# Kernel tuning notes

Measured on AMD Instinct MI355X. Metric: run time of the kernel, lower is better.

Reference implementation:

```python
import jax, jax.numpy as jnp
import numpy as np

N, E, H, NODE_IN, EDGE_DIM, L = 10000, 400000, 128, 6, 3, 4
LN_EPS = 1e-5


def _lin_init(key, fan_in, fan_out):
    return jax.random.normal(key, (fan_in, fan_out), dtype=jnp.float32) / np.sqrt(fan_in)


def setup_inputs() -> dict:
    key = jax.random.key(0)
    ks = jax.random.split(key, 24)
    x = jax.random.normal(ks[0], (N, NODE_IN), dtype=jnp.float32)
    edge_index = jax.random.randint(ks[1], (2, E), 0, N, dtype=jnp.int64)
    edge_attr = jax.random.normal(ks[2], (E, EDGE_DIM), dtype=jnp.float32)
    # encoder
    enc_w1 = _lin_init(ks[3], NODE_IN, H); enc_b1 = jnp.zeros((H,), jnp.float32)
    enc_w2 = _lin_init(ks[4], H, H); enc_b2 = jnp.zeros((H,), jnp.float32)
    # per-layer stacked params [L, ...]
    msg_w1 = jax.vmap(lambda k: _lin_init(k, 2 * H + EDGE_DIM, H))(jax.random.split(ks[5], L))
    msg_b1 = jnp.zeros((L, H), jnp.float32)
    msg_w2 = jax.vmap(lambda k: _lin_init(k, H, H))(jax.random.split(ks[6], L))
    msg_b2 = jnp.zeros((L, H), jnp.float32)
    upd_w1 = jax.vmap(lambda k: _lin_init(k, 2 * H, H))(jax.random.split(ks[7], L))
    upd_b1 = jnp.zeros((L, H), jnp.float32)
    upd_w2 = jax.vmap(lambda k: _lin_init(k, H, H))(jax.random.split(ks[8], L))
    upd_b2 = jnp.zeros((L, H), jnp.float32)
    ln_g = jnp.ones((L, H), jnp.float32)
    ln_b = jnp.zeros((L, H), jnp.float32)
    # decoder
    dec_w1 = _lin_init(ks[9], H, H); dec_b1 = jnp.zeros((H,), jnp.float32)
    dec_w2 = _lin_init(ks[10], H, 1); dec_b2 = jnp.zeros((1,), jnp.float32)
    return dict(x=x, edge_index=edge_index, edge_attr=edge_attr,
                enc_w1=enc_w1, enc_b1=enc_b1, enc_w2=enc_w2, enc_b2=enc_b2,
                msg_w1=msg_w1, msg_b1=msg_b1, msg_w2=msg_w2, msg_b2=msg_b2,
                upd_w1=upd_w1, upd_b1=upd_b1, upd_w2=upd_w2, upd_b2=upd_b2,
                ln_g=ln_g, ln_b=ln_b,
                dec_w1=dec_w1, dec_b1=dec_b1, dec_w2=dec_w2, dec_b2=dec_b2)


def _layernorm(h, g, b):
    mu = jnp.mean(h, axis=-1, keepdims=True)
    var = jnp.mean(jnp.square(h - mu), axis=-1, keepdims=True)
    return (h - mu) * jax.lax.rsqrt(var + LN_EPS) * g + b


def reference(x, edge_index, edge_attr,
              enc_w1, enc_b1, enc_w2, enc_b2,
              msg_w1, msg_b1, msg_w2, msg_b2,
              upd_w1, upd_b1, upd_w2, upd_b2,
              ln_g, ln_b,
              dec_w1, dec_b1, dec_w2, dec_b2):
    src, tgt = edge_index[0], edge_index[1]  # PyG default flow: message from x_j=src to x_i=tgt
    # in-degree counts for mean aggregation (zero-degree nodes -> 0 output, like scatter_mean)
    counts = jax.ops.segment_sum(jnp.ones((E,), jnp.float32), tgt, num_segments=N)
    inv_counts = (1.0 / jnp.maximum(counts, 1.0))[:, None]
    # encoder
    h = jax.nn.relu(x @ enc_w1 + enc_b1) @ enc_w2 + enc_b2  # [N, H]
    for l in range(L):
        x_i = h[tgt]  # [E, H] target features
        x_j = h[src]  # [E, H] source features
        m_in = jnp.concatenate([x_i, x_j, edge_attr], axis=-1)  # [E, 2H+edge_dim]
        m = jax.nn.relu(m_in @ msg_w1[l] + msg_b1[l]) @ msg_w2[l] + msg_b2[l]  # [E, H]
        agg = jax.ops.segment_sum(m, tgt, num_segments=N) * inv_counts  # [N, H] mean aggregate
        u_in = jnp.concatenate([h, agg], axis=-1)  # [N, 2H]
        u = jax.nn.relu(u_in @ upd_w1[l] + upd_b1[l]) @ upd_w2[l] + upd_b2[l]
        h = _layernorm(u + h, ln_g[l], ln_b[l])  # residual (in==out channels)
    # decoder
    return jax.nn.relu(h @ dec_w1 + dec_b1) @ dec_w2 + dec_b2  # [N, 1]
```

## Files before the change

kernel.cpp:

```cpp
#include <hip/hip_runtime.h>

#define NN 10000
#define NE 400000
#define HD 128
#define NIN 6
#define EDIM 3
#define NL 4
#define CAP 96
#define LN_EPS 1e-5f

typedef unsigned short u16;
using short8 = __attribute__((ext_vector_type(8))) short;
using f32x4 = __attribute__((ext_vector_type(4))) float;

__device__ __forceinline__ u16 f2bf(float x) {
    unsigned u = __float_as_uint(x);
    return (u16)((u + 0x7fff + ((u >> 16) & 1)) >> 16);
}
__device__ __forceinline__ float bf2f(u16 h) { return __uint_as_float(((unsigned)h) << 16); }
__device__ __forceinline__ void split2(float x, u16& hi, u16& lo) {
    hi = f2bf(x);
    lo = f2bf(x - bf2f(hi));
}
#define MFMA(a, b, c) __builtin_amdgcn_mfma_f32_16x16x32_bf16((a), (b), (c), 0, 0, 0)


__global__ __launch_bounds__(256) void k_prep(
    const float* __restrict__ msg_w2, const float* __restrict__ msg_b2, const float* __restrict__ upd_w1,
    const float* __restrict__ upd_w2, const float* __restrict__ msg_w1, const float* __restrict__ dec_w1,
    const float* __restrict__ enc_w2, float* __restrict__ M2, float* __restrict__ c2, int* __restrict__ cnt,
    u16* __restrict__ fG2, u16* __restrict__ fPQ, u16* __restrict__ fDec, u16* __restrict__ fEnc) {
    int idx = blockIdx.x * 256 + threadIdx.x;
    if (idx < 65536) {
        int l = idx >> 14, rem = idx & 16383, i = rem >> 7, jj = rem & 127;
        const float* U1b = upd_w1 + (size_t)l * 2 * HD * HD + (size_t)HD * HD;
        const float* W2 = msg_w2 + (size_t)l * HD * HD + (size_t)i * HD;
        float acc = 0.f;
        for (int t = 0; t < HD; ++t) acc += W2[t] * U1b[(size_t)t * HD + jj];
        M2[idx] = acc;
    } else if (idx < 66048) {
        int r = idx - 65536;
        int l = r >> 7, jj = r & 127;
        const float* U1b = upd_w1 + (size_t)l * 2 * HD * HD + (size_t)HD * HD;
        const float* b2 = msg_b2 + l * HD;
        float acc = 0.f;
        for (int t = 0; t < HD; ++t) acc += b2[t] * U1b[(size_t)t * HD + jj];
        c2[r] = acc;
    } else if (idx < 76048) {
        cnt[idx - 66048] = 0;
    } else if (idx < 84240) {
        int gg = idx - 76048;
        int l = gg >> 11, r = gg & 2047;
        int ct = r >> 8, ks = (r >> 6) & 3, lane = r & 63;
        int n = ct * 16 + (lane & 15), kb = ks * 32 + ((lane >> 4) << 3);
        u16* dst = fG2 + (size_t)gg * 8;
        const float* W = upd_w2 + (size_t)l * 128 * 128;
#pragma unroll
        for (int j = 0; j < 8; ++j) dst[j] = f2bf(W[(size_t)(kb + j) * 128 + n]);
    } else if (idx < 100624) {
        int gg = idx - 84240;
        int li = gg >> 12, r = gg & 4095;
        int ct = r >> 8, ks = (r >> 6) & 3, lane = r & 63;
        int n = ct * 16 + (lane & 15), kb = ks * 32 + ((lane >> 4) << 3);
        u16* dst = fPQ + (size_t)gg * 8;
        const float* W = msg_w1 + (size_t)li * (2 * HD + EDIM) * HD;
#pragma unroll
        for (int j = 0; j < 8; ++j) {
            int k = kb + j;
            float v = (n < 128) ? W[(size_t)k * 128 + n] : W[(size_t)(128 + k) * 128 + (n - 128)];
            dst[j] = f2bf(v);
        }
    } else if (idx < 102672) {
        int r = idx - 100624;
        int ct = r >> 8, ks = (r >> 6) & 3, lane = r & 63;
        int n = ct * 16 + (lane & 15), kb = ks * 32 + ((lane >> 4) << 3);
        u16* dst = fDec + (size_t)r * 8;
#pragma unroll
        for (int j = 0; j < 8; ++j) dst[j] = f2bf(dec_w1[(size_t)(kb + j) * 128 + n]);
    } else if (idx < 104720) {
        int r = idx - 102672;
        int ct = r >> 8, ks = (r >> 6) & 3, lane = r & 63;
        int n = ct * 16 + (lane & 15), kb = ks * 32 + ((lane >> 4) << 3);
        u16* dst = fEnc + (size_t)r * 8;
#pragma unroll
        for (int j = 0; j < 8; ++j) dst[j] = f2bf(enc_w2[(size_t)(kb + j) * 128 + n]);
    }
}


__global__ __launch_bounds__(256) void k_scatfrag(
    const int* __restrict__ src, const int* __restrict__ tgt, const float* __restrict__ ea,
    int* __restrict__ cnt, float4* __restrict__ sea,
    const float* __restrict__ upd_w1, const float* __restrict__ M2, u16* __restrict__ fG1) {
    if (blockIdx.x < 64) {
        int g = blockIdx.x * 256 + threadIdx.x;
        int l = g >> 12, r = g & 4095;
        int ct = r >> 9, ks = (r >> 6) & 7, lane = r & 63;
        int n = ct * 16 + (lane & 15), kb = ks * 32 + ((lane >> 4) << 3);
        u16* dst = fG1 + (size_t)g * 8;
        const float* U = upd_w1 + (size_t)l * 256 * 128;
        const float* Ml = M2 + (size_t)l * 128 * 128;
#pragma unroll
        for (int j = 0; j < 8; ++j) {
            int k = kb + j;
            float v = (k < 128) ? U[(size_t)k * 128 + n] : Ml[(size_t)(k - 128) * 128 + n];
            dst[j] = f2bf(v);
        }
    } else {
        int e = (blockIdx.x - 64) * 256 + threadIdx.x;
        if (e >= NE) return;
        int t = tgt[e];
        int pos = atomicAdd(&cnt[t], 1);
        if (pos < CAP) {
            sea[t * CAP + pos] =
                make_float4(ea[e * 3], ea[e * 3 + 1], ea[e * 3 + 2], __uint_as_float((unsigned)src[e]));
        }
    }
}


__global__ __launch_bounds__(512) void k_enc(const float* __restrict__ x, const float* __restrict__ ew1,
                                             const float* __restrict__ eb1, const u16* __restrict__ fEnc,
                                             const float* __restrict__ eb2, const u16* __restrict__ fPQ0,
                                             const float* __restrict__ mb1, u16* __restrict__ h_hi,
                                             u16* __restrict__ h_lo, float* __restrict__ PQf,
                                             u16* __restrict__ Qb) {
    __shared__ u16 tHi[2048], tLo[2048];
    int tid = threadIdx.x, w = tid >> 6, lane = tid & 63, q = lane >> 4, c = lane & 15;
    int band = blockIdx.x * 16;
    {
        int col = w * 16 + c;
        float wv[NIN];
#pragma unroll
        for (int k = 0; k < NIN; ++k) wv[k] = ew1[k * HD + col];
        float ebv = eb1[col];
#pragma unroll
        for (int reg = 0; reg < 4; ++reg) {
            int row = band + q * 4 + reg;
            float t = ebv;
#pragma unroll
            for (int k = 0; k < NIN; ++k) t += x[(size_t)row * NIN + k] * wv[k];
            t = fmaxf(t, 0.f);
            u16 hi, lo;
            split2(t, hi, lo);
            int r16 = q * 4 + reg;
            int a = r16 * 128 + (((col >> 3) ^ r16) << 3) + (col & 7);
            tHi[a] = hi;
            tLo[a] = lo;
        }
    }
    __syncthreads();
    short8 aH[4], aL[4];
#pragma unroll
    for (int ks = 0; ks < 4; ++ks) {
        int a = c * 128 + (((ks * 4 + q) ^ c) << 3);
        aH[ks] = *(const short8*)&tHi[a];
        aL[ks] = *(const short8*)&tLo[a];
    }
    f32x4 acc = {0, 0, 0, 0};
    {
        const u16* fb = fEnc + (size_t)w * 4 * 512 + lane * 8;
#pragma unroll
        for (int ks = 0; ks < 4; ++ks) {
            short8 b = *(const short8*)(fb + ks * 512);
            acc = MFMA(aH[ks], b, acc);
            acc = MFMA(aL[ks], b, acc);
        }
    }
    __syncthreads();
    {
        int col = w * 16 + c;
        float ebv = eb2[col];
#pragma unroll
        for (int reg = 0; reg < 4; ++reg) {
            int r16 = q * 4 + reg, row = band + r16;
            float hval = acc[reg] + ebv;
            u16 hi, lo;
            split2(hval, hi, lo);
            h_hi[(size_t)row * HD + col] = hi;
            h_lo[(size_t)row * HD + col] = lo;
            int a = r16 * 128 + (((col >> 3) ^ r16) << 3) + (col & 7);
            tHi[a] = hi;
            tLo[a] = lo;
        }
    }
    __syncthreads();
#pragma unroll
    for (int ks = 0; ks < 4; ++ks) {
        int a = c * 128 + (((ks * 4 + q) ^ c) << 3);
        aH[ks] = *(const short8*)&tHi[a];
        aL[ks] = *(const short8*)&tLo[a];
    }
#pragma unroll
    for (int i = 0; i < 2; ++i) {
        int ctg = w * 2 + i;
        const u16* fb = fPQ0 + (size_t)ctg * 4 * 512 + lane * 8;
        f32x4 a3 = {0, 0, 0, 0};
#pragma unroll
        for (int ks = 0; ks < 4; ++ks) {
            short8 b = *(const short8*)(fb + ks * 512);
            a3 = MFMA(aH[ks], b, a3);
            a3 = MFMA(aL[ks], b, a3);
        }
        int col = ctg * 16 + c;
        if (ctg < 8) {
            float bias = mb1[col];
#pragma unroll
            for (int reg = 0; reg < 4; ++reg)
                PQf[(size_t)(band + q * 4 + reg) * HD + col] = a3[reg] + bias;
        } else {
            int colq = col - 128;
#pragma unroll
            for (int reg = 0; reg < 4; ++reg)
                Qb[(size_t)(band + q * 4 + reg) * HD + colq] = f2bf(a3[reg]);
        }
    }
}


template <bool LAST>
__global__ __launch_bounds__(512) void k_layer(
    const float* __restrict__ PQf_in, const u16* __restrict__ Qb_in,
    const int* __restrict__ cnt, const float4* __restrict__ sea, const float* __restrict__ wc,
    u16* __restrict__ h_hi, u16* __restrict__ h_lo,
    const u16* __restrict__ fG1, const u16* __restrict__ fG2,
    const float* __restrict__ ub1, const float* __restrict__ c2l, const float* __restrict__ ub2,
    const float* __restrict__ g, const float* __restrict__ bb,
    const u16* __restrict__ fPQ, const float* __restrict__ nb1,
    float* __restrict__ PQf_out, u16* __restrict__ Qb_out,
    const u16* __restrict__ fDec, const float* __restrict__ db1, const float* __restrict__ dw2,
    const float* __restrict__ db2, float* __restrict__ out) {
    __shared__ u16 sHi[2048], sLo[2048];
    __shared__ u16 tHi[2048], tLo[2048];
    __shared__ float red[8][8][2];
    int tid = threadIdx.x, w = tid >> 6, lane = tid & 63, q = lane >> 4, c = lane & 15;
    int band = blockIdx.x * 8;
    int j = lane * 2;
    {
        float2 wcr0 = *(const float2*)(wc + j);
        float2 wcr1 = *(const float2*)(wc + HD + j);
        float2 wcr2 = *(const float2*)(wc + 2 * HD + j);
        int n = __builtin_amdgcn_readfirstlane(band + w);
        int cn = cnt[n];
        float invn = 1.0f / fmaxf((float)cn, 1.0f);
        int cle = __builtin_amdgcn_readfirstlane(cn < CAP ? cn : CAP);
        float2 p = *(const float2*)(PQf_in + (size_t)n * HD + j);
        float acc0 = 0.f, acc1 = 0.f;
        const float4* bucket = sea + (size_t)n * CAP;
        auto edge1 = [&](float4 A) {
            int sv = (int)__float_as_uint(A.w);
            float c0 = A.x * wcr0.x + A.y * wcr1.x + A.z * wcr2.x;
            float c1 = A.x * wcr0.y + A.y * wcr1.y + A.z * wcr2.y;
            unsigned u = *(const unsigned*)(Qb_in + (size_t)sv * HD + j);
            acc0 += fmaxf(p.x + __uint_as_float(u << 16) + c0, 0.f);
            acc1 += fmaxf(p.y + __uint_as_float(u & 0xffff0000u) + c1, 0.f);
        };
        int e = 0;
        for (; e + 3 < cle; e += 4) {
            float4 A0 = bucket[e], A1 = bucket[e + 1], A2 = bucket[e + 2], A3 = bucket[e + 3];
            edge1(A0);
            edge1(A1);
            edge1(A2);
            edge1(A3);
        }
        for (; e < cle; ++e) edge1(bucket[e]);
        float v0 = acc0 * invn, v1 = acc1 * invn;
        u16 h0, l0, h1, l1;
        split2(v0, h0, l0);
        split2(v1, h1, l1);
        int a = w * 128 + (((j >> 3) ^ w) << 3) + (j & 7);
        *(ushort2*)&sHi[a] = make_ushort2(h0, h1);
        *(ushort2*)&sLo[a] = make_ushort2(l0, l1);
    }
    __syncthreads();
    f32x4 acc = {0, 0, 0, 0};
    {
        const u16* fb = fG1 + (size_t)w * 8 * 512 + lane * 8;
        size_t rb = (size_t)(band + c) * HD + q * 8;
#pragma unroll
        for (int ks = 0; ks < 4; ++ks) {
            short8 aH = *(const short8*)(h_hi + rb + ks * 32);
            short8 aL = *(const short8*)(h_lo + rb + ks * 32);
            short8 b = *(const short8*)(fb + ks * 512);
            acc = MFMA(aH, b, acc);
            acc = MFMA(aL, b, acc);
        }
#pragma unroll
        for (int ks = 0; ks < 4; ++ks) {
            int a = c * 128 + (((ks * 4 + q) ^ c) << 3);
            short8 aH = *(const short8*)&sHi[a];
            short8 aL = *(const short8*)&sLo[a];
            short8 b = *(const short8*)(fb + (4 + ks) * 512);
            acc = MFMA(aH, b, acc);
            acc = MFMA(aL, b, acc);
        }
    }
    float alv[4];
#pragma unroll
    for (int reg = 0; reg < 4; ++reg) alv[reg] = (cnt[band + ((q * 4 + reg) & 7)] > 0) ? 1.f : 0.f;
    {
        int col = w * 16 + c;
        float u1b = ub1[col], cc = c2l[col];
#pragma unroll
        for (int reg = 0; reg < 4; ++reg) {
            int r16 = q * 4 + reg;
            float t = fmaxf(acc[reg] + u1b + alv[reg] * cc, 0.f);
            u16 hi, lo;
            split2(t, hi, lo);
            int a = r16 * 128 + (((col >> 3) ^ r16) << 3) + (col & 7);
            tHi[a] = hi;
            tLo[a] = lo;
        }
    }
    __syncthreads();
    f32x4 acc2 = {0, 0, 0, 0};
    {
        const u16* fb = fG2 + (size_t)w * 4 * 512 + lane * 8;
#pragma unroll
        for (int ks = 0; ks < 4; ++ks) {
            int a = c * 128 + (((ks * 4 + q) ^ c) << 3);
            short8 aH = *(const short8*)&tHi[a];
            short8 aL = *(const short8*)&tLo[a];
            short8 b = *(const short8*)(fb + ks * 512);
            acc2 = MFMA(aH, b, acc2);
            acc2 = MFMA(aL, b, acc2);
        }
    }
    float vv[4];
    {
        int col = w * 16 + c;
        float u2b = ub2[col];
#pragma unroll
        for (int reg = 0; reg < 4; ++reg) {
            int r16 = q * 4 + reg;
            size_t idx = (size_t)(band + (r16 & 7)) * HD + col;
            float hres = bf2f(h_hi[idx]) + bf2f(h_lo[idx]);
            vv[reg] = acc2[reg] + u2b + hres;
        }
    }
#pragma unroll
    for (int reg = 0; reg < 4; ++reg) {
        float s = vv[reg];
        float s2 = vv[reg] * vv[reg];
        for (int m = 1; m < 16; m <<= 1) {
            s += __shfl_xor(s, m);
            s2 += __shfl_xor(s2, m);
        }
        int r16 = q * 4 + reg;
        if (c == 0 && r16 < 8) {
            red[r16][w][0] = s;
            red[r16][w][1] = s2;
        }
    }
    __syncthreads();
    float mu[4], rs[4];
#pragma unroll
    for (int reg = 0; reg < 4; ++reg) {
        int r16 = q * 4 + reg;
        if (r16 < 8) {
            float S1 = 0.f, S2 = 0.f;
#pragma unroll
            for (int ww = 0; ww < 8; ++ww) {
                S1 += red[r16][ww][0];
                S2 += red[r16][ww][1];
            }
            float m = S1 * (1.f / HD);
            float var = S2 * (1.f / HD) - m * m;
            mu[reg] = m;
            rs[reg] = rsqrtf(var + LN_EPS);
        } else {
            mu[reg] = 0.f;
            rs[reg] = 1.f;
        }
    }
    {
        int col = w * 16 + c;
        float gg = g[col], bv = bb[col];
#pragma unroll
        for (int reg = 0; reg < 4; ++reg) {
            int r16 = q * 4 + reg;
            float o = (vv[reg] - mu[reg]) * rs[reg] * gg + bv;
            u16 hi, lo;
            split2(o, hi, lo);
            int a = r16 * 128 + (((col >> 3) ^ r16) << 3) + (col & 7);
            tHi[a] = hi;
            tLo[a] = lo;
            if (!LAST && r16 < 8) {
                size_t idx = (size_t)(band + r16) * HD + col;
                h_hi[idx] = hi;
                h_lo[idx] = lo;
            }
        }
    }
    __syncthreads();
    short8 aH3[4], aL3[4];
#pragma unroll
    for (int ks = 0; ks < 4; ++ks) {
        int a = c * 128 + (((ks * 4 + q) ^ c) << 3);
        aH3[ks] = *(const short8*)&tHi[a];
        aL3[ks] = *(const short8*)&tLo[a];
    }
    if (!LAST) {
#pragma unroll
        for (int i = 0; i < 2; ++i) {
            int ctg = w * 2 + i;
            const u16* fb = fPQ + (size_t)ctg * 4 * 512 + lane * 8;
            f32x4 a3 = {0, 0, 0, 0};
#pragma unroll
            for (int ks = 0; ks < 4; ++ks) {
                short8 b = *(const short8*)(fb + ks * 512);
                a3 = MFMA(aH3[ks], b, a3);
                a3 = MFMA(aL3[ks], b, a3);
            }
            int col = ctg * 16 + c;
            if (ctg < 8) {
                float bias = nb1[col];
#pragma unroll
                for (int reg = 0; reg < 4; ++reg) {
                    int r16 = q * 4 + reg;
                    if (r16 < 8) PQf_out[(size_t)(band + r16) * HD + col] = a3[reg] + bias;
                }
            } else {
                int colq = col - 128;
#pragma unroll
                for (int reg = 0; reg < 4; ++reg) {
                    int r16 = q * 4 + reg;
                    if (r16 < 8) Qb_out[(size_t)(band + r16) * HD + colq] = f2bf(a3[reg]);
                }
            }
        }
    } else {
        float part[4];
        {
            const u16* fb = fDec + (size_t)w * 4 * 512 + lane * 8;
            f32x4 a3 = {0, 0, 0, 0};
#pragma unroll
            for (int ks = 0; ks < 4; ++ks) {
                short8 b = *(const short8*)(fb + ks * 512);
                a3 = MFMA(aH3[ks], b, a3);
                a3 = MFMA(aL3[ks], b, a3);
            }
            int col = w * 16 + c;
            float w2v = dw2[col], b1v = db1[col];
#pragma unroll
            for (int reg = 0; reg < 4; ++reg) part[reg] = fmaxf(a3[reg] + b1v, 0.f) * w2v;
        }
#pragma unroll
        for (int reg = 0; reg < 4; ++reg) {
            float s = part[reg];
            for (int m = 1; m < 16; m <<= 1) s += __shfl_xor(s, m);
            int r16 = q * 4 + reg;
            if (c == 0 && r16 < 8) red[r16][w][0] = s;
        }
        __syncthreads();
        if (tid < 8) {
            float s = db2[0];
#pragma unroll
            for (int ww = 0; ww < 8; ++ww) s += red[tid][ww][0];
            out[band + tid] = s;
        }
    }
}


extern "C" void kernel_launch(void* const* d_in, const int* in_sizes, int n_in,
                              void* d_out, int out_size, void* d_ws, size_t ws_size,
                              hipStream_t stream) {
    const float* x = (const float*)d_in[0];
    const int* eidx = (const int*)d_in[1];
    const float* eattr = (const float*)d_in[2];
    const float* enc_w1 = (const float*)d_in[3];
    const float* enc_b1 = (const float*)d_in[4];
    const float* enc_w2 = (const float*)d_in[5];
    const float* enc_b2 = (const float*)d_in[6];
    const float* msg_w1 = (const float*)d_in[7];
    const float* msg_b1 = (const float*)d_in[8];
    const float* msg_w2 = (const float*)d_in[9];
    const float* msg_b2 = (const float*)d_in[10];
    const float* upd_w1 = (const float*)d_in[11];
    const float* upd_b1 = (const float*)d_in[12];
    const float* upd_w2 = (const float*)d_in[13];
    const float* upd_b2 = (const float*)d_in[14];
    const float* ln_g = (const float*)d_in[15];
    const float* ln_b = (const float*)d_in[16];
    const float* dec_w1 = (const float*)d_in[17];
    const float* dec_b1 = (const float*)d_in[18];
    const float* dec_w2 = (const float*)d_in[19];
    const float* dec_b2 = (const float*)d_in[20];
    const int* srcp = eidx;
    const int* tgtp = eidx + NE;

    char* base = (char*)d_ws;
    size_t off = 0;
    auto alloc = [&](size_t bytes) -> void* {
        off = (off + 15) & ~(size_t)15;
        void* p = base + off;
        off += bytes;
        return p;
    };
    float4* sea = (float4*)alloc((size_t)NN * CAP * 16);
    float* PQf0 = (float*)alloc((size_t)NN * HD * 4);
    float* PQf1 = (float*)alloc((size_t)NN * HD * 4);
    u16* Qb0 = (u16*)alloc((size_t)NN * HD * 2);
    u16* Qb1 = (u16*)alloc((size_t)NN * HD * 2);
    u16* h_hi = (u16*)alloc((size_t)NN * HD * 2);
    u16* h_lo = (u16*)alloc((size_t)NN * HD * 2);
    int* cnt = (int*)alloc((size_t)NN * 4);
    float* M2 = (float*)alloc((size_t)NL * HD * HD * 4);
    float* c2 = (float*)alloc((size_t)NL * HD * 4);
    u16* fG1 = (u16*)alloc((size_t)131072 * 2);
    u16* fG2 = (u16*)alloc((size_t)65536 * 2);
    u16* fPQ = (u16*)alloc((size_t)131072 * 2);
    u16* fDec = (u16*)alloc((size_t)16384 * 2);
    u16* fEnc = (u16*)alloc((size_t)16384 * 2);

    k_prep<<<410, 256, 0, stream>>>(msg_w2, msg_b2, upd_w1, upd_w2, msg_w1, dec_w1, enc_w2,
                                    M2, c2, cnt, fG2, fPQ, fDec, fEnc);
    k_scatfrag<<<64 + (NE + 255) / 256, 256, 0, stream>>>(srcp, tgtp, eattr, cnt, sea, upd_w1, M2, fG1);
    k_enc<<<NN / 16, 512, 0, stream>>>(x, enc_w1, enc_b1, fEnc, enc_b2, fPQ, msg_b1, h_hi, h_lo, PQf0, Qb0);

    float* PQin = PQf0;
    u16* Qin = Qb0;
    float* PQout = PQf1;
    u16* Qout = Qb1;
    for (int l = 0; l < NL; ++l) {
        const float* wc = msg_w1 + (size_t)l * (2 * HD + EDIM) * HD + (size_t)2 * HD * HD;
        if (l < NL - 1) {
            k_layer<false><<<NN / 8, 512, 0, stream>>>(
                PQin, Qin, cnt, sea, wc, h_hi, h_lo,
                fG1 + (size_t)l * 32768, fG2 + (size_t)l * 16384,
                upd_b1 + l * HD, c2 + l * HD, upd_b2 + l * HD, ln_g + l * HD, ln_b + l * HD,
                fPQ + (size_t)(l + 1) * 32768, msg_b1 + (size_t)(l + 1) * HD, PQout, Qout,
                nullptr, nullptr, nullptr, nullptr, nullptr);
        } else {
            k_layer<true><<<NN / 8, 512, 0, stream>>>(
                PQin, Qin, cnt, sea, wc, h_hi, h_lo,
                fG1 + (size_t)l * 32768, fG2 + (size_t)l * 16384,
                upd_b1 + l * HD, c2 + l * HD, upd_b2 + l * HD, ln_g + l * HD, ln_b + l * HD,
                nullptr, nullptr, nullptr, nullptr,
                fDec, dec_b1, dec_w2, dec_b2, (float*)d_out);
        }
        float* tf = PQin; PQin = PQout; PQout = tf;
        u16* tq = Qin; Qin = Qout; Qout = tq;
    }
}
```

Before: 310.7 us.

## Process 16 nodes per layer block with split-edge gather per wave

Each layer block now handles 16 nodes instead of 8, so all 16 rows of the 16x16 MFMA tiles hold real data and the row masks go away. Each wave aggregates two nodes; within a wave the two 32-lane halves take alternate edges, each lane reads 4 columns, and the halves are combined with a cross-half shuffle. The aim is to stop wasting half of every MFMA tile and to make the gather loads wider and more parallel. In exchange, the grid is half as large, which lowers occupancy and the number of blocks available to hide gather latency.

```diff
diff --git a/kernel.cpp b/kernel.cpp
--- a/kernel.cpp
+++ b/kernel.cpp
@@ -232,45 +232,77 @@
     const float* __restrict__ db2, float* __restrict__ out) {
     __shared__ u16 sHi[2048], sLo[2048];
     __shared__ u16 tHi[2048], tLo[2048];
-    __shared__ float red[8][8][2];
+    __shared__ float red[16][8][2];
     int tid = threadIdx.x, w = tid >> 6, lane = tid & 63, q = lane >> 4, c = lane & 15;
-    int band = blockIdx.x * 8;
-    int j = lane * 2;
-    {
-        float2 wcr0 = *(const float2*)(wc + j);
-        float2 wcr1 = *(const float2*)(wc + HD + j);
-        float2 wcr2 = *(const float2*)(wc + 2 * HD + j);
-        int n = __builtin_amdgcn_readfirstlane(band + w);
-        int cn = cnt[n];
-        float invn = 1.0f / fmaxf((float)cn, 1.0f);
-        int cle = __builtin_amdgcn_readfirstlane(cn < CAP ? cn : CAP);
-        float2 p = *(const float2*)(PQf_in + (size_t)n * HD + j);
-        float acc0 = 0.f, acc1 = 0.f;
-        const float4* bucket = sea + (size_t)n * CAP;
-        auto edge1 = [&](float4 A) {
-            int sv = (int)__float_as_uint(A.w);
-            float c0 = A.x * wcr0.x + A.y * wcr1.x + A.z * wcr2.x;
-            float c1 = A.x * wcr0.y + A.y * wcr1.y + A.z * wcr2.y;
-            unsigned u = *(const unsigned*)(Qb_in + (size_t)sv * HD + j);
-            acc0 += fmaxf(p.x + __uint_as_float(u << 16) + c0, 0.f);
-            acc1 += fmaxf(p.y + __uint_as_float(u & 0xffff0000u) + c1, 0.f);
-        };
-        int e = 0;
-        for (; e + 3 < cle; e += 4) {
-            float4 A0 = bucket[e], A1 = bucket[e + 1], A2 = bucket[e + 2], A3 = bucket[e + 3];
-            edge1(A0);
-            edge1(A1);
-            edge1(A2);
-            edge1(A3);
-        }
-        for (; e < cle; ++e) edge1(bucket[e]);
-        float v0 = acc0 * invn, v1 = acc1 * invn;
-        u16 h0, l0, h1, l1;
-        split2(v0, h0, l0);
-        split2(v1, h1, l1);
-        int a = w * 128 + (((j >> 3) ^ w) << 3) + (j & 7);
-        *(ushort2*)&sHi[a] = make_ushort2(h0, h1);
-        *(ushort2*)&sLo[a] = make_ushort2(l0, l1);
+    int band = blockIdx.x * 16;
+    {
+        int half = lane >> 5;
+        int lc = lane & 31;
+        int col0 = lc * 4;
+        float4 wcr0 = *(const float4*)(wc + col0);
+        float4 wcr1 = *(const float4*)(wc + HD + col0);
+        float4 wcr2 = *(const float4*)(wc + 2 * HD + col0);
+#pragma unroll
+        for (int i = 0; i < 2; ++i) {
+            int r16 = w * 2 + i;
+            int n = __builtin_amdgcn_readfirstlane(band + r16);
+            int cn = cnt[n];
+            float invn = 1.0f / fmaxf((float)cn, 1.0f);
+            int cle = __builtin_amdgcn_readfirstlane(cn < CAP ? cn : CAP);
+            float4 p = *(const float4*)(PQf_in + (size_t)n * HD + col0);
+            f32x4 acc = {0, 0, 0, 0};
+            const float4* bucket = sea + (size_t)n * CAP;
+            auto edge1 = [&](float4 A, ushort4 qv) {
+                float c0 = A.x * wcr0.x + A.y * wcr1.x + A.z * wcr2.x;
+                float c1 = A.x * wcr0.y + A.y * wcr1.y + A.z * wcr2.y;
+                float c2v = A.x * wcr0.z + A.y * wcr1.z + A.z * wcr2.z;
+                float c3 = A.x * wcr0.w + A.y * wcr1.w + A.z * wcr2.w;
+                acc[0] += fmaxf(p.x + bf2f(qv.x) + c0, 0.f);
+                acc[1] += fmaxf(p.y + bf2f(qv.y) + c1, 0.f);
+                acc[2] += fmaxf(p.z + bf2f(qv.z) + c2v, 0.f);
+                acc[3] += fmaxf(p.w + bf2f(qv.w) + c3, 0.f);
+            };
+            int nit = cle >> 1;
+            int it = 0;
+            for (; it + 4 <= nit; it += 4) {
+                float4 A0 = bucket[2 * (it + 0) + half];
+                float4 A1 = bucket[2 * (it + 1) + half];
+                float4 A2 = bucket[2 * (it + 2) + half];
+                float4 A3 = bucket[2 * (it + 3) + half];
+                ushort4 q0 = *(const ushort4*)(Qb_in + (size_t)__float_as_uint(A0.w) * HD + col0);
+                ushort4 q1 = *(const ushort4*)(Qb_in + (size_t)__float_as_uint(A1.w) * HD + col0);
+                ushort4 q2 = *(const ushort4*)(Qb_in + (size_t)__float_as_uint(A2.w) * HD + col0);
+                ushort4 q3 = *(const ushort4*)(Qb_in + (size_t)__float_as_uint(A3.w) * HD + col0);
+                edge1(A0, q0);
+                edge1(A1, q1);
+                edge1(A2, q2);
+                edge1(A3, q3);
+            }
+            for (; it < nit; ++it) {
+                float4 A0 = bucket[2 * it + half];
+                ushort4 q0 = *(const ushort4*)(Qb_in + (size_t)__float_as_uint(A0.w) * HD + col0);
+                edge1(A0, q0);
+            }
+            if ((cle & 1) && half == 0) {
+                float4 A0 = bucket[cle - 1];
+                ushort4 q0 = *(const ushort4*)(Qb_in + (size_t)__float_as_uint(A0.w) * HD + col0);
+                edge1(A0, q0);
+            }
+#pragma unroll
+            for (int k = 0; k < 4; ++k) acc[k] += __shfl_xor(acc[k], 32);
+            if (lane < 32) {
+                ushort4 hi4, lo4;
+                float v0 = acc[0] * invn, v1 = acc[1] * invn, v2 = acc[2] * invn, v3 = acc[3] * invn;
+                split2(v0, hi4.x, lo4.x);
+                split2(v1, hi4.y, lo4.y);
+                split2(v2, hi4.z, lo4.z);
+                split2(v3, hi4.w, lo4.w);
+                int chunk = (lc >> 1) ^ r16;
+                int a = r16 * 128 + (chunk << 3) + 4 * (lc & 1);
+                *(ushort4*)&sHi[a] = hi4;
+                *(ushort4*)&sLo[a] = lo4;
+            }
+        }
     }
     __syncthreads();
     f32x4 acc = {0, 0, 0, 0};
@@ -279,25 +311,25 @@
         size_t rb = (size_t)(band + c) * HD + q * 8;
 #pragma unroll
         for (int ks = 0; ks < 4; ++ks) {
-            short8 aH = *(const short8*)(h_hi + rb + ks * 32);
-            short8 aL = *(const short8*)(h_lo + rb + ks * 32);
+            short8 aHh = *(const short8*)(h_hi + rb + ks * 32);
+            short8 aLl = *(const short8*)(h_lo + rb + ks * 32);
             short8 b = *(const short8*)(fb + ks * 512);
-            acc = MFMA(aH, b, acc);
-            acc = MFMA(aL, b, acc);
+            acc = MFMA(aHh, b, acc);
+            acc = MFMA(aLl, b, acc);
         }
 #pragma unroll
         for (int ks = 0; ks < 4; ++ks) {
             int a = c * 128 + (((ks * 4 + q) ^ c) << 3);
-            short8 aH = *(const short8*)&sHi[a];
-            short8 aL = *(const short8*)&sLo[a];
+            short8 aHh = *(const short8*)&sHi[a];
+            short8 aLl = *(const short8*)&sLo[a];
             short8 b = *(const short8*)(fb + (4 + ks) * 512);
-            acc = MFMA(aH, b, acc);
-            acc = MFMA(aL, b, acc);
+            acc = MFMA(aHh, b, acc);
+            acc = MFMA(aLl, b, acc);
         }
     }
     float alv[4];
 #pragma unroll
-    for (int reg = 0; reg < 4; ++reg) alv[reg] = (cnt[band + ((q * 4 + reg) & 7)] > 0) ? 1.f : 0.f;
+    for (int reg = 0; reg < 4; ++reg) alv[reg] = (cnt[band + q * 4 + reg] > 0) ? 1.f : 0.f;
     {
         int col = w * 16 + c;
         float u1b = ub1[col], cc = c2l[col];
@@ -319,11 +351,11 @@
 #pragma unroll
         for (int ks = 0; ks < 4; ++ks) {
             int a = c * 128 + (((ks * 4 + q) ^ c) << 3);
-            short8 aH = *(const short8*)&tHi[a];
-            short8 aL = *(const short8*)&tLo[a];
+            short8 aHh = *(const short8*)&tHi[a];
+            short8 aLl = *(const short8*)&tLo[a];
             short8 b = *(const short8*)(fb + ks * 512);
-            acc2 = MFMA(aH, b, acc2);
-            acc2 = MFMA(aL, b, acc2);
+            acc2 = MFMA(aHh, b, acc2);
+            acc2 = MFMA(aLl, b, acc2);
         }
     }
     float vv[4];
@@ -332,8 +364,7 @@
         float u2b = ub2[col];
 #pragma unroll
         for (int reg = 0; reg < 4; ++reg) {
-            int r16 = q * 4 + reg;
-            size_t idx = (size_t)(band + (r16 & 7)) * HD + col;
+            size_t idx = (size_t)(band + q * 4 + reg) * HD + col;
             float hres = bf2f(h_hi[idx]) + bf2f(h_lo[idx]);
             vv[reg] = acc2[reg] + u2b + hres;
         }
@@ -346,10 +377,9 @@
             s += __shfl_xor(s, m);
             s2 += __shfl_xor(s2, m);
         }
-        int r16 = q * 4 + reg;
-        if (c == 0 && r16 < 8) {
-            red[r16][w][0] = s;
-            red[r16][w][1] = s2;
+        if (c == 0) {
+            red[q * 4 + reg][w][0] = s;
+            red[q * 4 + reg][w][1] = s2;
         }
     }
     __syncthreads();
@@ -357,21 +387,16 @@
 #pragma unroll
     for (int reg = 0; reg < 4; ++reg) {
         int r16 = q * 4 + reg;
-        if (r16 < 8) {
-            float S1 = 0.f, S2 = 0.f;
-#pragma unroll
-            for (int ww = 0; ww < 8; ++ww) {
-                S1 += red[r16][ww][0];
-                S2 += red[r16][ww][1];
-            }
-            float m = S1 * (1.f / HD);
-            float var = S2 * (1.f / HD) - m * m;
-            mu[reg] = m;
-            rs[reg] = rsqrtf(var + LN_EPS);
-        } else {
-            mu[reg] = 0.f;
-            rs[reg] = 1.f;
-        }
+        float S1 = 0.f, S2 = 0.f;
+#pragma unroll
+        for (int ww = 0; ww < 8; ++ww) {
+            S1 += red[r16][ww][0];
+            S2 += red[r16][ww][1];
+        }
+        float m = S1 * (1.f / HD);
+        float var = S2 * (1.f / HD) - m * m;
+        mu[reg] = m;
+        rs[reg] = rsqrtf(var + LN_EPS);
     }
     {
         int col = w * 16 + c;
@@ -385,7 +410,7 @@
             int a = r16 * 128 + (((col >> 3) ^ r16) << 3) + (col & 7);
             tHi[a] = hi;
             tLo[a] = lo;
-            if (!LAST && r16 < 8) {
+            if (!LAST) {
                 size_t idx = (size_t)(band + r16) * HD + col;
                 h_hi[idx] = hi;
                 h_lo[idx] = lo;
@@ -416,17 +441,13 @@
             if (ctg < 8) {
                 float bias = nb1[col];
 #pragma unroll
-                for (int reg = 0; reg < 4; ++reg) {
-                    int r16 = q * 4 + reg;
-                    if (r16 < 8) PQf_out[(size_t)(band + r16) * HD + col] = a3[reg] + bias;
-                }
+                for (int reg = 0; reg < 4; ++reg)
+                    PQf_out[(size_t)(band + q * 4 + reg) * HD + col] = a3[reg] + bias;
             } else {
                 int colq = col - 128;
 #pragma unroll
-                for (int reg = 0; reg < 4; ++reg) {
-                    int r16 = q * 4 + reg;
-                    if (r16 < 8) Qb_out[(size_t)(band + r16) * HD + colq] = f2bf(a3[reg]);
-                }
+                for (int reg = 0; reg < 4; ++reg)
+                    Qb_out[(size_t)(band + q * 4 + reg) * HD + colq] = f2bf(a3[reg]);
             }
         }
     } else {
@@ -449,11 +470,10 @@
         for (int reg = 0; reg < 4; ++reg) {
             float s = part[reg];
             for (int m = 1; m < 16; m <<= 1) s += __shfl_xor(s, m);
-            int r16 = q * 4 + reg;
-            if (c == 0 && r16 < 8) red[r16][w][0] = s;
+            if (c == 0) red[q * 4 + reg][w][0] = s;
         }
         __syncthreads();
-        if (tid < 8) {
+        if (tid < 16) {
             float s = db2[0];
 #pragma unroll
             for (int ww = 0; ww < 8; ++ww) s += red[tid][ww][0];
@@ -526,14 +546,14 @@
     for (int l = 0; l < NL; ++l) {
         const float* wc = msg_w1 + (size_t)l * (2 * HD + EDIM) * HD + (size_t)2 * HD * HD;
         if (l < NL - 1) {
-            k_layer<false><<<NN / 8, 512, 0, stream>>>(
+            k_layer<false><<<NN / 16, 512, 0, stream>>>(
                 PQin, Qin, cnt, sea, wc, h_hi, h_lo,
                 fG1 + (size_t)l * 32768, fG2 + (size_t)l * 16384,
                 upd_b1 + l * HD, c2 + l * HD, upd_b2 + l * HD, ln_g + l * HD, ln_b + l * HD,
                 fPQ + (size_t)(l + 1) * 32768, msg_b1 + (size_t)(l + 1) * HD, PQout, Qout,
                 nullptr, nullptr, nullptr, nullptr, nullptr);
         } else {
-            k_layer<true><<<NN / 8, 512, 0, stream>>>(
+            k_layer<true><<<NN / 16, 512, 0, stream>>>(
                 PQin, Qin, cnt, sea, wc, h_hi, h_lo,
                 fG1 + (size_t)l * 32768, fG2 + (size_t)l * 16384,
                 upd_b1 + l * HD, c2 + l * HD, upd_b2 + l * HD, ln_g + l * HD, ln_b + l * HD,
```

New measurement: 309.9 us. Within noise of the previous version (-0.3%).
